# Performance work log

Hardware: AMD Instinct MI355X
Metric: run time of the kernel (lower is better)

Reference implementation:

```python
import jax, jax.numpy as jnp
import numpy as np

# int64 required: hash primes (2654435761) * coord ints overflow int32; torch uses int64.
jax.config.update("jax_enable_x64", True)

N_LEVELS = 16
F_PER_LEVEL = 2
TABLE_SIZE = 2 ** 19
BASE_RES = 16
FINEST_RES = 512
N_POINTS = 1_000_000


def _level_resolutions():
    # matches: floor(base * exp(level * log(finest/base) / (L-1)))
    g = np.log(FINEST_RES / BASE_RES) / (N_LEVELS - 1)
    return np.floor(BASE_RES * np.exp(np.arange(N_LEVELS) * g)).astype(np.float32)


def setup_inputs() -> dict:
    key = jax.random.key(0)
    k1, k2 = jax.random.split(key)
    coords = jax.random.uniform(k1, (N_POINTS, 3), dtype=jnp.float32)  # points in [0,1)^3
    tables = jax.random.uniform(k2, (N_LEVELS, TABLE_SIZE, F_PER_LEVEL),
                                dtype=jnp.float32, minval=-1e-4, maxval=1e-4)
    return {"coords": coords, "tables": tables}


def _forward(coords, tables):
    primes = jnp.array([1, 2654435761, 805459861], dtype=jnp.int64)
    # corner offset order matches the i,j,k nested loops in the source
    offsets = jnp.array([[i, j, k] for i in (0, 1) for j in (0, 1) for k in (0, 1)],
                        dtype=jnp.float32)  # [8,3]
    resolutions = jnp.asarray(_level_resolutions())  # [L]

    def level_fn(table, res):
        scaled = coords * res                      # [N,3]
        floor = jnp.floor(scaled)
        frac = scaled - floor                      # [N,3]
        corners = floor[:, None, :] + offsets      # [N,8,3]
        # faithful to source hash_coords: corners are scaled by resolution AGAIN before hashing
        ci = (corners * res).astype(jnp.int64)     # trunc toward zero; coords >= 0
        h = (ci * primes).sum(-1) % TABLE_SIZE     # [N,8]
        cf = table[h]                              # [N,8,F] gather
        x = frac[:, 0:1]; y = frac[:, 1:2]; z = frac[:, 2:3]
        c00 = cf[:, 0] * (1 - x) + cf[:, 4] * x
        c01 = cf[:, 1] * (1 - x) + cf[:, 5] * x
        c10 = cf[:, 2] * (1 - x) + cf[:, 6] * x
        c11 = cf[:, 3] * (1 - x) + cf[:, 7] * x
        c0 = c00 * (1 - y) + c10 * y
        c1 = c01 * (1 - y) + c11 * y
        return c0 * (1 - z) + c1 * z               # [N,F]

    feats = jax.vmap(level_fn)(tables, resolutions)       # [L,N,F]
    # concat over levels along feature dim, level-major order
    return jnp.transpose(feats, (1, 0, 2)).reshape(coords.shape[0], N_LEVELS * F_PER_LEVEL)


def reference(coords, tables):
    return _forward(coords, tables)
```

## Files before the change

### kernel.cpp

```cpp
#include <hip/hip_runtime.h>

#define HG_LEVELS 16
#define HG_TMASK ((1u << 19) - 1u)
#define HG_P2 2654435761u
#define HG_P3 805459861u

__device__ __constant__ float kResF[HG_LEVELS] = {
    16.f, 20.f, 25.f, 32.f, 40.f, 50.f, 64.f, 80.f,
    101.f, 128.f, 161.f, 203.f, 256.f, 322.f, 406.f, 512.f};

__global__ __launch_bounds__(256) void hg_gather(
    const float* __restrict__ coords,
    const float* __restrict__ tables,
    float2* __restrict__ ws,
    int n, int lbase) {
  const int b = blockIdx.x;
  const int l = lbase + (b & 7);
  const int p = ((b >> 3) << 8) + (int)threadIdx.x;
  if (p >= n) return;

  const float x = coords[3 * p + 0];
  const float y = coords[3 * p + 1];
  const float z = coords[3 * p + 2];

  const float r = kResF[l];
  const uint ri = (uint)r;
  const uint rp2 = ri * HG_P2;
  const uint rp3 = ri * HG_P3;
  const float2* __restrict__ tb =
      reinterpret_cast<const float2*>(tables) + ((size_t)l << 19);

  const float sx = x * r, sy = y * r, sz = z * r;
  const float fx = floorf(sx), fy = floorf(sy), fz = floorf(sz);
  const float wx = sx - fx, wy = sy - fy, wz = sz - fz;

  const uint hx0 = (uint)(fx * r);
  const uint hx1 = hx0 + ri;
  const uint hy0 = (uint)(fy * r) * HG_P2;
  const uint hy1 = hy0 + rp2;
  const uint hz0 = (uint)(fz * r) * HG_P3;
  const uint hz1 = hz0 + rp3;

  const uint h0 = (hx0 + hy0 + hz0) & HG_TMASK;
  const uint h1 = (hx0 + hy0 + hz1) & HG_TMASK;
  const uint h2 = (hx0 + hy1 + hz0) & HG_TMASK;
  const uint h3 = (hx0 + hy1 + hz1) & HG_TMASK;
  const uint h4 = (hx1 + hy0 + hz0) & HG_TMASK;
  const uint h5 = (hx1 + hy0 + hz1) & HG_TMASK;
  const uint h6 = (hx1 + hy1 + hz0) & HG_TMASK;
  const uint h7 = (hx1 + hy1 + hz1) & HG_TMASK;

  const float2 c0 = tb[h0];
  const float2 c1 = tb[h1];
  const float2 c2 = tb[h2];
  const float2 c3 = tb[h3];
  const float2 c4 = tb[h4];
  const float2 c5 = tb[h5];
  const float2 c6 = tb[h6];
  const float2 c7 = tb[h7];

  const float ox = 1.f - wx, oy = 1.f - wy, oz = 1.f - wz;

  float2 f;
  {
    const float c00 = c0.x * ox + c4.x * wx;
    const float c01 = c1.x * ox + c5.x * wx;
    const float c10 = c2.x * ox + c6.x * wx;
    const float c11 = c3.x * ox + c7.x * wx;
    const float d0 = c00 * oy + c10 * wy;
    const float d1 = c01 * oy + c11 * wy;
    f.x = d0 * oz + d1 * wz;
  }
  {
    const float c00 = c0.y * ox + c4.y * wx;
    const float c01 = c1.y * ox + c5.y * wx;
    const float c10 = c2.y * ox + c6.y * wx;
    const float c11 = c3.y * ox + c7.y * wx;
    const float d0 = c00 * oy + c10 * wy;
    const float d1 = c01 * oy + c11 * wy;
    f.y = d0 * oz + d1 * wz;
  }

  ws[l * n + p] = f;
}

__global__ __launch_bounds__(256, 4) void hg_transpose(
    const float2* __restrict__ ws, float* __restrict__ out, int n) {
  __shared__ float s[256 * 33];
  const int tid = threadIdx.x;
  const int p0 = blockIdx.x << 8;
  const int p = p0 + tid;
  if (p < n) {
#pragma unroll
    for (int l = 0; l < HG_LEVELS; ++l) {
      const float2 v = ws[l * n + p];
      s[tid * 33 + 2 * l + 0] = v.x;
      s[tid * 33 + 2 * l + 1] = v.y;
    }
  }
  __syncthreads();
  const int outbase = p0 * 32;
  const int lim = n * 32;
#pragma unroll
  for (int k = 0; k < 32; ++k) {
    const int flat = (k << 8) + tid;
    const int idx = outbase + flat;
    if (idx < lim) out[idx] = s[(flat >> 5) * 33 + (flat & 31)];
  }
}

__global__ __launch_bounds__(256, 4) void hashgrid_fwd(
    const float* __restrict__ coords, const float* __restrict__ tables,
    float* __restrict__ out, int n) {
  constexpr float RES[HG_LEVELS] = {
      16.f, 20.f, 25.f, 32.f, 40.f, 50.f, 64.f, 80.f,
      101.f, 128.f, 161.f, 203.f, 256.f, 322.f, 406.f, 512.f};
  __shared__ float sout[256 * 33];
  const int tid = threadIdx.x;
  const int p0 = blockIdx.x << 8;
  const int p = p0 + tid;
  float x = 0.f, y = 0.f, z = 0.f;
  if (p < n) {
    x = coords[3 * p + 0];
    y = coords[3 * p + 1];
    z = coords[3 * p + 2];
  }
#pragma unroll
  for (int l = 0; l < HG_LEVELS; ++l) {
    const float r = RES[l];
    const uint ri = (uint)RES[l];
    const uint rp2 = ri * HG_P2;
    const uint rp3 = ri * HG_P3;
    const float2* __restrict__ tb =
        reinterpret_cast<const float2*>(tables) + ((size_t)l << 19);
    const float sx = x * r, sy = y * r, sz = z * r;
    const float fx = floorf(sx), fy = floorf(sy), fz = floorf(sz);
    const float wx = sx - fx, wy = sy - fy, wz = sz - fz;
    const uint hx0 = (uint)(fx * r);
    const uint hx1 = hx0 + ri;
    const uint hy0 = (uint)(fy * r) * HG_P2;
    const uint hy1 = hy0 + rp2;
    const uint hz0 = (uint)(fz * r) * HG_P3;
    const uint hz1 = hz0 + rp3;
    const float2 c0 = tb[(hx0 + hy0 + hz0) & HG_TMASK];
    const float2 c1 = tb[(hx0 + hy0 + hz1) & HG_TMASK];
    const float2 c2 = tb[(hx0 + hy1 + hz0) & HG_TMASK];
    const float2 c3 = tb[(hx0 + hy1 + hz1) & HG_TMASK];
    const float2 c4 = tb[(hx1 + hy0 + hz0) & HG_TMASK];
    const float2 c5 = tb[(hx1 + hy0 + hz1) & HG_TMASK];
    const float2 c6 = tb[(hx1 + hy1 + hz0) & HG_TMASK];
    const float2 c7 = tb[(hx1 + hy1 + hz1) & HG_TMASK];
    const float ox = 1.f - wx, oy = 1.f - wy, oz = 1.f - wz;
    float f0, f1;
    {
      const float c00 = c0.x * ox + c4.x * wx;
      const float c01 = c1.x * ox + c5.x * wx;
      const float c10 = c2.x * ox + c6.x * wx;
      const float c11 = c3.x * ox + c7.x * wx;
      f0 = (c00 * oy + c10 * wy) * oz + (c01 * oy + c11 * wy) * wz;
    }
    {
      const float c00 = c0.y * ox + c4.y * wx;
      const float c01 = c1.y * ox + c5.y * wx;
      const float c10 = c2.y * ox + c6.y * wx;
      const float c11 = c3.y * ox + c7.y * wx;
      f1 = (c00 * oy + c10 * wy) * oz + (c01 * oy + c11 * wy) * wz;
    }
    sout[tid * 33 + 2 * l + 0] = f0;
    sout[tid * 33 + 2 * l + 1] = f1;
  }
  __syncthreads();
  const int outbase = p0 * 32;
  const int lim = n * 32;
#pragma unroll
  for (int k = 0; k < 32; ++k) {
    const int flat = (k << 8) + tid;
    const int idx = outbase + flat;
    if (idx < lim) out[idx] = sout[(flat >> 5) * 33 + (flat & 31)];
  }
}

extern "C" void kernel_launch(void* const* d_in, const int* in_sizes, int n_in,
                              void* d_out, int out_size, void* d_ws,
                              size_t ws_size, hipStream_t stream) {
  const float* coords = (const float*)d_in[0];
  const float* tables = (const float*)d_in[1];
  float* out = (float*)d_out;
  const int n = in_sizes[0] / 3;
  const int npb = (n + 255) / 256;

  const size_t need = (size_t)HG_LEVELS * (size_t)n * sizeof(float2);
  if (ws_size >= need) {
    float2* ws = (float2*)d_ws;
    hipLaunchKernelGGL(hg_gather, dim3(npb * 8), dim3(256), 0, stream,
                       coords, tables, ws, n, 0);
    hipLaunchKernelGGL(hg_gather, dim3(npb * 8), dim3(256), 0, stream,
                       coords, tables, ws, n, 8);
    hipLaunchKernelGGL(hg_transpose, dim3(npb), dim3(256), 0, stream,
                       ws, out, n);
  } else {
    hipLaunchKernelGGL(hashgrid_fwd, dim3(npb), dim3(256), 0, stream,
                       coords, tables, out, n);
  }
}
```

Measured before the change: 765.4 us.

## Pack z-neighbor table entries into float4 to halve random gathers

Adds a pre-pass that builds, per level, a packed table where each entry holds its own features plus those of the entry offset by the z-prime hash delta. The gather kernel then fetches four 16-byte corners instead of eight 8-byte corners, cutting random memory transactions. The cost is an extra pass reading the tables and writing a double-size packed copy each call, plus a larger workspace requirement. Nontemporal stores/loads are also used for the intermediate and output buffers.

```diff
diff --git a/kernel.cpp b/kernel.cpp
--- a/kernel.cpp
+++ b/kernel.cpp
@@ -1,19 +1,36 @@
 #include <hip/hip_runtime.h>
 
 #define HG_LEVELS 16
-#define HG_TMASK ((1u << 19) - 1u)
+#define HG_M (1u << 19)
+#define HG_TMASK (HG_M - 1u)
 #define HG_P2 2654435761u
 #define HG_P3 805459861u
+
+typedef float f32x2 __attribute__((ext_vector_type(2)));
+typedef float f32x4 __attribute__((ext_vector_type(4)));
 
 __device__ __constant__ float kResF[HG_LEVELS] = {
     16.f, 20.f, 25.f, 32.f, 40.f, 50.f, 64.f, 80.f,
     101.f, 128.f, 161.f, 203.f, 256.f, 322.f, 406.f, 512.f};
 
-__global__ __launch_bounds__(256) void hg_gather(
-    const float* __restrict__ coords,
-    const float* __restrict__ tables,
-    float2* __restrict__ ws,
-    int n, int lbase) {
+__global__ __launch_bounds__(256) void hg_build(
+    const float* __restrict__ tables, f32x4* __restrict__ packed) {
+  const int l = blockIdx.x >> 11;
+  const uint m = ((blockIdx.x & 2047u) << 8) | threadIdx.x;
+  const uint ri = (uint)kResF[l];
+  const uint d3 = (ri * HG_P3) & HG_TMASK;
+  const f32x2* __restrict__ tb =
+      reinterpret_cast<const f32x2*>(tables) + ((size_t)l << 19);
+  const f32x2 a = tb[m];
+  const f32x2 b = tb[(m + d3) & HG_TMASK];
+  f32x4 v;
+  v.x = a.x; v.y = a.y; v.z = b.x; v.w = b.y;
+  __builtin_nontemporal_store(v, &packed[((size_t)l << 19) + m]);
+}
+
+__global__ __launch_bounds__(256) void hg_gather_p(
+    const float* __restrict__ coords, const f32x4* __restrict__ packed,
+    f32x2* __restrict__ feats, int n, int lbase) {
   const int b = blockIdx.x;
   const int l = lbase + (b & 7);
   const int p = ((b >> 3) << 8) + (int)threadIdx.x;
@@ -26,87 +43,125 @@
   const float r = kResF[l];
   const uint ri = (uint)r;
   const uint rp2 = ri * HG_P2;
-  const uint rp3 = ri * HG_P3;
-  const float2* __restrict__ tb =
-      reinterpret_cast<const float2*>(tables) + ((size_t)l << 19);
+  const f32x4* __restrict__ tb = packed + ((size_t)l << 19);
 
   const float sx = x * r, sy = y * r, sz = z * r;
   const float fx = floorf(sx), fy = floorf(sy), fz = floorf(sz);
   const float wx = sx - fx, wy = sy - fy, wz = sz - fz;
 
+  const uint hx0 = (uint)(fx * r);
+  const uint hy0 = (uint)(fy * r) * HG_P2;
+  const uint hz0 = (uint)(fz * r) * HG_P3;
+  const uint base = hx0 + hy0 + hz0;
+
+  const uint m00 = base & HG_TMASK;
+  const uint m01 = (base + rp2) & HG_TMASK;
+  const uint m10 = (base + ri) & HG_TMASK;
+  const uint m11 = (base + ri + rp2) & HG_TMASK;
+
+  const f32x4 q00 = tb[m00];
+  const f32x4 q01 = tb[m01];
+  const f32x4 q10 = tb[m10];
+  const f32x4 q11 = tb[m11];
+
+  const float ox = 1.f - wx, oy = 1.f - wy, oz = 1.f - wz;
+
+  f32x2 f;
+  {
+    const float c00 = q00.x * ox + q10.x * wx;
+    const float c01 = q00.z * ox + q10.z * wx;
+    const float c10 = q01.x * ox + q11.x * wx;
+    const float c11 = q01.z * ox + q11.z * wx;
+    f.x = (c00 * oy + c10 * wy) * oz + (c01 * oy + c11 * wy) * wz;
+  }
+  {
+    const float c00 = q00.y * ox + q10.y * wx;
+    const float c01 = q00.w * ox + q10.w * wx;
+    const float c10 = q01.y * ox + q11.y * wx;
+    const float c11 = q01.w * ox + q11.w * wx;
+    f.y = (c00 * oy + c10 * wy) * oz + (c01 * oy + c11 * wy) * wz;
+  }
+
+  __builtin_nontemporal_store(f, &feats[(size_t)l * n + p]);
+}
+
+__global__ __launch_bounds__(256, 4) void hg_transpose(
+    const f32x2* __restrict__ feats, float* __restrict__ out, int n) {
+  __shared__ float s[256 * 33];
+  const int tid = threadIdx.x;
+  const int p0 = blockIdx.x << 8;
+  const int p = p0 + tid;
+  if (p < n) {
+#pragma unroll
+    for (int l = 0; l < HG_LEVELS; ++l) {
+      const f32x2 v = __builtin_nontemporal_load(&feats[(size_t)l * n + p]);
+      s[tid * 33 + 2 * l + 0] = v.x;
+      s[tid * 33 + 2 * l + 1] = v.y;
+    }
+  }
+  __syncthreads();
+  const int outbase = p0 * 32;
+  const int lim = n * 32;
+#pragma unroll
+  for (int k = 0; k < 32; ++k) {
+    const int flat = (k << 8) + tid;
+    const int idx = outbase + flat;
+    if (idx < lim)
+      __builtin_nontemporal_store(s[(flat >> 5) * 33 + (flat & 31)],
+                                  &out[idx]);
+  }
+}
+
+__global__ __launch_bounds__(256) void hg_gather(
+    const float* __restrict__ coords, const float* __restrict__ tables,
+    f32x2* __restrict__ ws, int n, int lbase) {
+  const int b = blockIdx.x;
+  const int l = lbase + (b & 7);
+  const int p = ((b >> 3) << 8) + (int)threadIdx.x;
+  if (p >= n) return;
+  const float x = coords[3 * p + 0];
+  const float y = coords[3 * p + 1];
+  const float z = coords[3 * p + 2];
+  const float r = kResF[l];
+  const uint ri = (uint)r;
+  const uint rp2 = ri * HG_P2;
+  const uint rp3 = ri * HG_P3;
+  const f32x2* __restrict__ tb =
+      reinterpret_cast<const f32x2*>(tables) + ((size_t)l << 19);
+  const float sx = x * r, sy = y * r, sz = z * r;
+  const float fx = floorf(sx), fy = floorf(sy), fz = floorf(sz);
+  const float wx = sx - fx, wy = sy - fy, wz = sz - fz;
   const uint hx0 = (uint)(fx * r);
   const uint hx1 = hx0 + ri;
   const uint hy0 = (uint)(fy * r) * HG_P2;
   const uint hy1 = hy0 + rp2;
   const uint hz0 = (uint)(fz * r) * HG_P3;
   const uint hz1 = hz0 + rp3;
-
-  const uint h0 = (hx0 + hy0 + hz0) & HG_TMASK;
-  const uint h1 = (hx0 + hy0 + hz1) & HG_TMASK;
-  const uint h2 = (hx0 + hy1 + hz0) & HG_TMASK;
-  const uint h3 = (hx0 + hy1 + hz1) & HG_TMASK;
-  const uint h4 = (hx1 + hy0 + hz0) & HG_TMASK;
-  const uint h5 = (hx1 + hy0 + hz1) & HG_TMASK;
-  const uint h6 = (hx1 + hy1 + hz0) & HG_TMASK;
-  const uint h7 = (hx1 + hy1 + hz1) & HG_TMASK;
-
-  const float2 c0 = tb[h0];
-  const float2 c1 = tb[h1];
-  const float2 c2 = tb[h2];
-  const float2 c3 = tb[h3];
-  const float2 c4 = tb[h4];
-  const float2 c5 = tb[h5];
-  const float2 c6 = tb[h6];
-  const float2 c7 = tb[h7];
-
+  const f32x2 c0 = tb[(hx0 + hy0 + hz0) & HG_TMASK];
+  const f32x2 c1 = tb[(hx0 + hy0 + hz1) & HG_TMASK];
+  const f32x2 c2 = tb[(hx0 + hy1 + hz0) & HG_TMASK];
+  const f32x2 c3 = tb[(hx0 + hy1 + hz1) & HG_TMASK];
+  const f32x2 c4 = tb[(hx1 + hy0 + hz0) & HG_TMASK];
+  const f32x2 c5 = tb[(hx1 + hy0 + hz1) & HG_TMASK];
+  const f32x2 c6 = tb[(hx1 + hy1 + hz0) & HG_TMASK];
+  const f32x2 c7 = tb[(hx1 + hy1 + hz1) & HG_TMASK];
   const float ox = 1.f - wx, oy = 1.f - wy, oz = 1.f - wz;
-
-  float2 f;
+  f32x2 f;
   {
     const float c00 = c0.x * ox + c4.x * wx;
     const float c01 = c1.x * ox + c5.x * wx;
     const float c10 = c2.x * ox + c6.x * wx;
     const float c11 = c3.x * ox + c7.x * wx;
-    const float d0 = c00 * oy + c10 * wy;
-    const float d1 = c01 * oy + c11 * wy;
-    f.x = d0 * oz + d1 * wz;
+    f.x = (c00 * oy + c10 * wy) * oz + (c01 * oy + c11 * wy) * wz;
   }
   {
     const float c00 = c0.y * ox + c4.y * wx;
     const float c01 = c1.y * ox + c5.y * wx;
     const float c10 = c2.y * ox + c6.y * wx;
     const float c11 = c3.y * ox + c7.y * wx;
-    const float d0 = c00 * oy + c10 * wy;
-    const float d1 = c01 * oy + c11 * wy;
-    f.y = d0 * oz + d1 * wz;
-  }
-
-  ws[l * n + p] = f;
-}
-
-__global__ __launch_bounds__(256, 4) void hg_transpose(
-    const float2* __restrict__ ws, float* __restrict__ out, int n) {
-  __shared__ float s[256 * 33];
-  const int tid = threadIdx.x;
-  const int p0 = blockIdx.x << 8;
-  const int p = p0 + tid;
-  if (p < n) {
-#pragma unroll
-    for (int l = 0; l < HG_LEVELS; ++l) {
-      const float2 v = ws[l * n + p];
-      s[tid * 33 + 2 * l + 0] = v.x;
-      s[tid * 33 + 2 * l + 1] = v.y;
-    }
-  }
-  __syncthreads();
-  const int outbase = p0 * 32;
-  const int lim = n * 32;
-#pragma unroll
-  for (int k = 0; k < 32; ++k) {
-    const int flat = (k << 8) + tid;
-    const int idx = outbase + flat;
-    if (idx < lim) out[idx] = s[(flat >> 5) * 33 + (flat & 31)];
-  }
+    f.y = (c00 * oy + c10 * wy) * oz + (c01 * oy + c11 * wy) * wz;
+  }
+  __builtin_nontemporal_store(f, &ws[(size_t)l * n + p]);
 }
 
 __global__ __launch_bounds__(256, 4) void hashgrid_fwd(
@@ -131,8 +186,8 @@
     const uint ri = (uint)RES[l];
     const uint rp2 = ri * HG_P2;
     const uint rp3 = ri * HG_P3;
-    const float2* __restrict__ tb =
-        reinterpret_cast<const float2*>(tables) + ((size_t)l << 19);
+    const f32x2* __restrict__ tb =
+        reinterpret_cast<const f32x2*>(tables) + ((size_t)l << 19);
     const float sx = x * r, sy = y * r, sz = z * r;
     const float fx = floorf(sx), fy = floorf(sy), fz = floorf(sz);
     const float wx = sx - fx, wy = sy - fy, wz = sz - fz;
@@ -142,14 +197,14 @@
     const uint hy1 = hy0 + rp2;
     const uint hz0 = (uint)(fz * r) * HG_P3;
     const uint hz1 = hz0 + rp3;
-    const float2 c0 = tb[(hx0 + hy0 + hz0) & HG_TMASK];
-    const float2 c1 = tb[(hx0 + hy0 + hz1) & HG_TMASK];
-    const float2 c2 = tb[(hx0 + hy1 + hz0) & HG_TMASK];
-    const float2 c3 = tb[(hx0 + hy1 + hz1) & HG_TMASK];
-    const float2 c4 = tb[(hx1 + hy0 + hz0) & HG_TMASK];
-    const float2 c5 = tb[(hx1 + hy0 + hz1) & HG_TMASK];
-    const float2 c6 = tb[(hx1 + hy1 + hz0) & HG_TMASK];
-    const float2 c7 = tb[(hx1 + hy1 + hz1) & HG_TMASK];
+    const f32x2 c0 = tb[(hx0 + hy0 + hz0) & HG_TMASK];
+    const f32x2 c1 = tb[(hx0 + hy0 + hz1) & HG_TMASK];
+    const f32x2 c2 = tb[(hx0 + hy1 + hz0) & HG_TMASK];
+    const f32x2 c3 = tb[(hx0 + hy1 + hz1) & HG_TMASK];
+    const f32x2 c4 = tb[(hx1 + hy0 + hz0) & HG_TMASK];
+    const f32x2 c5 = tb[(hx1 + hy0 + hz1) & HG_TMASK];
+    const f32x2 c6 = tb[(hx1 + hy1 + hz0) & HG_TMASK];
+    const f32x2 c7 = tb[(hx1 + hy1 + hz1) & HG_TMASK];
     const float ox = 1.f - wx, oy = 1.f - wy, oz = 1.f - wz;
     float f0, f1;
     {
@@ -189,15 +244,28 @@
   const int n = in_sizes[0] / 3;
   const int npb = (n + 255) / 256;
 
-  const size_t need = (size_t)HG_LEVELS * (size_t)n * sizeof(float2);
-  if (ws_size >= need) {
-    float2* ws = (float2*)d_ws;
+  const size_t packed_bytes = (size_t)HG_LEVELS * HG_M * sizeof(f32x4);
+  const size_t feat_bytes = (size_t)HG_LEVELS * (size_t)n * sizeof(f32x2);
+
+  if (ws_size >= packed_bytes + feat_bytes) {
+    f32x4* packed = (f32x4*)d_ws;
+    f32x2* feats = (f32x2*)((char*)d_ws + packed_bytes);
+    hipLaunchKernelGGL(hg_build, dim3(HG_LEVELS * 2048), dim3(256), 0, stream,
+                       tables, packed);
+    hipLaunchKernelGGL(hg_gather_p, dim3(npb * 8), dim3(256), 0, stream,
+                       coords, packed, feats, n, 0);
+    hipLaunchKernelGGL(hg_gather_p, dim3(npb * 8), dim3(256), 0, stream,
+                       coords, packed, feats, n, 8);
+    hipLaunchKernelGGL(hg_transpose, dim3(npb), dim3(256), 0, stream,
+                       feats, out, n);
+  } else if (ws_size >= feat_bytes) {
+    f32x2* feats = (f32x2*)d_ws;
     hipLaunchKernelGGL(hg_gather, dim3(npb * 8), dim3(256), 0, stream,
-                       coords, tables, ws, n, 0);
+                       coords, tables, feats, n, 0);
     hipLaunchKernelGGL(hg_gather, dim3(npb * 8), dim3(256), 0, stream,
-                       coords, tables, ws, n, 8);
+                       coords, tables, feats, n, 8);
     hipLaunchKernelGGL(hg_transpose, dim3(npb), dim3(256), 0, stream,
-                       ws, out, n);
+                       feats, out, n);
   } else {
     hipLaunchKernelGGL(hashgrid_fwd, dim3(npb), dim3(256), 0, stream,
                        coords, tables, out, n);
```

After: 677.8 us. -11.4%, faster.
